# Performance work log

Hardware: AMD Instinct MI355X
Metric: run time of the kernel (lower is better)

Reference implementation:

```python
import jax, jax.numpy as jnp
import numpy as np

B, S, H = 1, 2048, 1024
NH, NKV, HD = 16, 4, 64  # n_attn_heads, n_kv_heads, head_dim


def setup_inputs() -> dict:
    key = jax.random.key(0)
    k1, k2, k3, k4 = jax.random.split(key, 4)
    x = jax.random.normal(k1, (B, S, H), dtype=jnp.float32)
    Wq = jax.random.normal(k2, (H, H), dtype=jnp.float32) * 0.02
    Wk = jax.random.normal(k3, (NKV * HD, H), dtype=jnp.float32) * 0.02
    Wv = jax.random.normal(k4, (NKV * HD, H), dtype=jnp.float32) * 0.02
    return {"x": x, "Wq": Wq, "Wk": Wk, "Wv": Wv}


def reference(x, Wq, Wk, Wv):
    b, s, h = x.shape
    rep = NH // NKV
    # projections (torch Linear: x @ W.T)
    q = (x @ Wq.T).reshape(b, s, NH, HD).transpose(0, 2, 1, 3)      # [b, NH, s, d]
    k = (x @ Wk.T).reshape(b, s, NKV, HD).transpose(0, 2, 1, 3)     # [b, NKV, s, d]
    v = (x @ Wv.T).reshape(b, s, NKV, HD).transpose(0, 2, 1, 3)
    # repeat_kv: expand each kv head rep times
    k = jnp.repeat(k, rep, axis=1)                                   # [b, NH, s, d]
    v = jnp.repeat(v, rep, axis=1)
    # NOTE: source scales by 1/sqrt(hidden_size), not 1/sqrt(head_dim)
    scale = 1.0 / np.sqrt(H).astype(np.float32)
    scores = jnp.einsum('bhqd,bhkd->bhqk', q, k) * scale             # [b, NH, s, s]
    causal = jnp.tril(jnp.ones((s, s), dtype=bool))
    scores = jnp.where(causal[None, None], scores, -jnp.inf)
    probs = jax.nn.softmax(scores, axis=-1)
    y = jnp.einsum('bhqk,bhkd->bhqd', probs, v)                      # [b, NH, s, d]
    return y.transpose(0, 2, 1, 3).reshape(b, s, NH * HD)
```

## Files before the change

### kernel.cpp

```cpp
#include <hip/hip_runtime.h>

#define S_LEN 2048
#define HID   1024
#define NHEAD 16
#define NKVH  4
#define HDIM  64
#define NPROJ 1536
#define QKSTR 1280

typedef __bf16 bf16x8 __attribute__((ext_vector_type(8)));
typedef __bf16 bf16x4 __attribute__((ext_vector_type(4)));
typedef float  f32x4  __attribute__((ext_vector_type(4)));
typedef short  s16x4  __attribute__((ext_vector_type(4)));

typedef const __attribute__((address_space(1))) void* gas_ptr;
typedef __attribute__((address_space(3))) void*       las_ptr;

#define QSCALE 0.04508422f

__device__ __forceinline__ unsigned short f2bf(float f) {
    unsigned u = __builtin_bit_cast(unsigned, f);
    u = u + 0x7FFFu + ((u >> 16) & 1u);
    return (unsigned short)(u >> 16);
}

__device__ __forceinline__ f32x4 mfma_16x16x16_bf16(s16x4 a, s16x4 b, f32x4 c) {
#if __has_builtin(__builtin_amdgcn_mfma_f32_16x16x16bf16_1k)
    return __builtin_amdgcn_mfma_f32_16x16x16bf16_1k(a, b, c, 0, 0, 0);
#else
    f32x4 d = c;
    asm volatile("s_nop 1\n\tv_mfma_f32_16x16x16_bf16 %0, %1, %2, %0\n\ts_nop 3"
                 : "+v"(d) : "v"(a), "v"(b));
    return d;
#endif
}

__global__ __launch_bounds__(256) void cvt_all(
    const float* __restrict__ x,  const float* __restrict__ wq,
    const float* __restrict__ wk, const float* __restrict__ wv,
    unsigned short* __restrict__ xbf, unsigned short* __restrict__ wbf)
{
    const long nx  = (long)S_LEN * HID;
    const long nwq = (long)HID * HID;
    const long nwk = (long)256 * HID;
    long i = (long)(blockIdx.x * 256 + threadIdx.x) * 4;
    const float* src; unsigned short* dst;
    if (i < nx)                  { src = x  + i;                 dst = xbf + i; }
    else if (i < nx + nwq)       { long j = i - nx;              src = wq + j; dst = wbf + j; }
    else if (i < nx + nwq + nwk) { long j = i - nx - nwq;        src = wk + j; dst = wbf + nwq + j; }
    else                         { long j = i - nx - nwq - nwk;  src = wv + j; dst = wbf + nwq + nwk + j; }
    float4 v = *(const float4*)src;
    ushort4 o; o.x = f2bf(v.x); o.y = f2bf(v.y); o.z = f2bf(v.z); o.w = f2bf(v.w);
    *(ushort4*)dst = o;
}

__global__ __launch_bounds__(256, 2) void proj_gemm(
    const unsigned short* __restrict__ xbf,
    const unsigned short* __restrict__ wbf,
    unsigned short* __restrict__ qkv,
    unsigned short* __restrict__ vT)
{
    __shared__ unsigned short At[2][64 * 64];
    __shared__ unsigned short Bt[2][96 * 64];
    const int tid = threadIdx.x;
    const int w = tid >> 6, l = tid & 63;
    const int quad = l >> 4, lane16 = l & 15;
    const int m0 = blockIdx.y * 64, n0 = blockIdx.x * 96;
    const int wm = (w & 1) * 32, wn = (w >> 1) * 48;

    const int srow = l >> 3;
    const int scol = ((l & 7) ^ srow) * 8;

    f32x4 acc[2][3] = {};

    #define STAGE(KT, BUF)                                                              \
        do {                                                                            \
            _Pragma("unroll")                                                           \
            for (int c = 0; c < 2; ++c) {                                               \
                const int rbase = w * 16 + c * 8;                                       \
                const unsigned short* ga =                                              \
                    xbf + (long)(m0 + rbase + srow) * HID + (KT) + scol;                \
                __builtin_amdgcn_global_load_lds((gas_ptr)ga,                           \
                    (las_ptr)&At[BUF][rbase * 64], 16, 0, 0);                           \
            }                                                                           \
            _Pragma("unroll")                                                           \
            for (int c = 0; c < 3; ++c) {                                               \
                const int rbase = w * 24 + c * 8;                                       \
                const unsigned short* gb =                                              \
                    wbf + (long)(n0 + rbase + srow) * HID + (KT) + scol;                \
                __builtin_amdgcn_global_load_lds((gas_ptr)gb,                           \
                    (las_ptr)&Bt[BUF][rbase * 64], 16, 0, 0);                           \
            }                                                                           \
        } while (0)

    STAGE(0, 0);

    for (int i = 0; i < 16; ++i) {
        const int cur = i & 1;
        __syncthreads();
        if (i + 1 < 16) STAGE((i + 1) * 64, cur ^ 1);

        #pragma unroll
        for (int ks = 0; ks < 2; ++ks) {
            const int swz = ((ks * 4 + quad) ^ (lane16 & 7)) * 8;
            bf16x8 a[2], b[3];
            #pragma unroll
            for (int mi = 0; mi < 2; ++mi)
                a[mi] = *(const bf16x8*)&At[cur][(wm + mi * 16 + lane16) * 64 + swz];
            #pragma unroll
            for (int ni = 0; ni < 3; ++ni)
                b[ni] = *(const bf16x8*)&Bt[cur][(wn + ni * 16 + lane16) * 64 + swz];
            #pragma unroll
            for (int mi = 0; mi < 2; ++mi)
                #pragma unroll
                for (int ni = 0; ni < 3; ++ni)
                    acc[mi][ni] = __builtin_amdgcn_mfma_f32_16x16x32_bf16(a[mi], b[ni], acc[mi][ni], 0, 0, 0);
        }
    }
    #undef STAGE

    #pragma unroll
    for (int mi = 0; mi < 2; ++mi) {
        const int row = m0 + wm + mi * 16 + quad * 4;
        #pragma unroll
        for (int ni = 0; ni < 3; ++ni) {
            const int col = n0 + wn + ni * 16 + lane16;
            #pragma unroll
            for (int r = 0; r < 4; ++r) {
                const float v = acc[mi][ni][r];
                if (col < 1024)
                    qkv[(long)(row + r) * QKSTR + col] = f2bf(v * QSCALE);
                else if (col < 1280)
                    qkv[(long)(row + r) * QKSTR + col] = f2bf(v);
                else
                    vT[(long)(col - 1280) * S_LEN + (row + r)] = f2bf(v);
            }
        }
    }
}

#define KSTR 72
__global__ __launch_bounds__(256, 2) void attn(
    const unsigned short* __restrict__ qkv,
    const unsigned short* __restrict__ vT,
    float* __restrict__ out)
{
    __shared__ unsigned short Kt[2][64 * KSTR];
    __shared__ unsigned short Vt[2][64 * KSTR];

    const int tid = threadIdx.x;
    const int w = tid >> 6, l = tid & 63;
    const int quad = l >> 4, lane16 = l & 15;
    const int bx = blockIdx.x, by = blockIdx.y;
    const int qt = (by & 8) ? (31 - bx) : bx;
    const int h  = by;
    const int kh = h >> 2;
    const int qcol = h * 64;
    const int kcol = 1024 + kh * 64;

    const long qrow = (long)(qt * 64 + w * 16 + lane16);
    bf16x8 qa0 = *(const bf16x8*)&qkv[qrow * QKSTR + qcol + quad * 8];
    bf16x8 qa1 = *(const bf16x8*)&qkv[qrow * QKSTR + qcol + 32 + quad * 8];

    f32x4 oT[4] = {};
    float rsum[4] = {0.f, 0.f, 0.f, 0.f};

    const int sr = tid >> 2, ss = tid & 3;
    const long vrow = (long)(kh * 64 + sr) * S_LEN;

    bf16x8 kr0, kr1, vr0, vr1;
    {
        const long gk = (long)sr * QKSTR + kcol + ss * 16;
        kr0 = *(const bf16x8*)&qkv[gk];
        kr1 = *(const bf16x8*)&qkv[gk + 8];
        const long gv = vrow + ss * 16;
        vr0 = *(const bf16x8*)&vT[gv];
        vr1 = *(const bf16x8*)&vT[gv + 8];
    }

    for (int kt = 0; kt <= qt; ++kt) {
        const int cur = kt & 1;
        *(bf16x8*)&Kt[cur][sr * KSTR + ss * 16]     = kr0;
        *(bf16x8*)&Kt[cur][sr * KSTR + ss * 16 + 8] = kr1;
        *(bf16x8*)&Vt[cur][sr * KSTR + ss * 16]     = vr0;
        *(bf16x8*)&Vt[cur][sr * KSTR + ss * 16 + 8] = vr1;

        __syncthreads();

        if (kt < qt) {
            const long gk = (long)((kt + 1) * 64 + sr) * QKSTR + kcol + ss * 16;
            kr0 = *(const bf16x8*)&qkv[gk];
            kr1 = *(const bf16x8*)&qkv[gk + 8];
            const long gv = vrow + (kt + 1) * 64 + ss * 16;
            vr0 = *(const bf16x8*)&vT[gv];
            vr1 = *(const bf16x8*)&vT[gv + 8];
        }

        f32x4 sacc[4] = {};
        __builtin_amdgcn_s_setprio(1);
        #pragma unroll
        for (int t = 0; t < 4; ++t) {
            bf16x8 kb0 = *(const bf16x8*)&Kt[cur][(t * 16 + lane16) * KSTR + quad * 8];
            bf16x8 kb1 = *(const bf16x8*)&Kt[cur][(t * 16 + lane16) * KSTR + 32 + quad * 8];
            sacc[t] = __builtin_amdgcn_mfma_f32_16x16x32_bf16(kb0, qa0, sacc[t], 0, 0, 0);
            sacc[t] = __builtin_amdgcn_mfma_f32_16x16x32_bf16(kb1, qa1, sacc[t], 0, 0, 0);
        }
        __builtin_amdgcn_s_setprio(0);

        if (kt == qt) {
            #pragma unroll
            for (int t = 0; t < 4; ++t) {
                const int kvw = t * 16 + quad * 4;
                #pragma unroll
                for (int r = 0; r < 4; ++r)
                    if (kvw + r > w * 16 + lane16) sacc[t][r] = -3.0e38f;
            }
        }

        s16x4 pfrag[4];
        #pragma unroll
        for (int t = 0; t < 4; ++t) {
            const float p0 = __builtin_amdgcn_exp2f(sacc[t][0]);
            const float p1 = __builtin_amdgcn_exp2f(sacc[t][1]);
            const float p2 = __builtin_amdgcn_exp2f(sacc[t][2]);
            const float p3 = __builtin_amdgcn_exp2f(sacc[t][3]);
            rsum[t] += (p0 + p1) + (p2 + p3);
            bf16x4 pk;
            pk[0] = (__bf16)p0; pk[1] = (__bf16)p1;
            pk[2] = (__bf16)p2; pk[3] = (__bf16)p3;
            pfrag[t] = __builtin_bit_cast(s16x4, pk);
        }

        __builtin_amdgcn_s_setprio(1);
        #pragma unroll
        for (int dt = 0; dt < 4; ++dt)
            #pragma unroll
            for (int t = 0; t < 4; ++t) {
                bf16x4 va = *(const bf16x4*)&Vt[cur][(dt * 16 + lane16) * KSTR + t * 16 + quad * 4];
                oT[dt] = mfma_16x16x16_bf16(__builtin_bit_cast(s16x4, va), pfrag[t], oT[dt]);
            }
        __builtin_amdgcn_s_setprio(0);
    }

    float total = (rsum[0] + rsum[1]) + (rsum[2] + rsum[3]);
    total += __shfl_xor(total, 16);
    total += __shfl_xor(total, 32);
    const float invt = 1.0f / total;

    const long orow_q = (long)(qt * 64 + w * 16 + lane16);
    #pragma unroll
    for (int dt = 0; dt < 4; ++dt) {
        const int col = h * 64 + dt * 16 + quad * 4;
        #pragma unroll
        for (int r = 0; r < 4; ++r)
            out[orow_q * (NHEAD * HDIM) + col + r] = oT[dt][r] * invt;
    }
}

extern "C" void kernel_launch(void* const* d_in, const int* in_sizes, int n_in,
                              void* d_out, int out_size, void* d_ws, size_t ws_size,
                              hipStream_t stream) {
    const float* x  = (const float*)d_in[0];
    const float* wq = (const float*)d_in[1];
    const float* wk = (const float*)d_in[2];
    const float* wv = (const float*)d_in[3];
    float* out = (float*)d_out;

    unsigned short* xbf = (unsigned short*)d_ws;
    unsigned short* wbf = xbf + (size_t)S_LEN * HID;
    unsigned short* qkv = wbf + (size_t)NPROJ * HID;
    unsigned short* vT  = qkv + (size_t)S_LEN * QKSTR;

    cvt_all<<<dim3(3584), dim3(256), 0, stream>>>(x, wq, wk, wv, xbf, wbf);
    proj_gemm<<<dim3(16, 32), dim3(256), 0, stream>>>(xbf, wbf, qkv, vT);
    attn<<<dim3(32, 16), dim3(256), 0, stream>>>(qkv, vT, out);
}
```

Measured before the change: 116.7 us.

## Fuse fp32-to-bf16 conversion into projection GEMM and process two KV tiles per barrier

Removes the separate conversion kernel. The projection GEMM now loads fp32 x and weights straight into registers, converts them to bf16 and writes them to shared memory, which saves a kernel launch and a round trip through the workspace. The attention kernel widens its shared K/V buffers to four slots and handles two 64-row KV tiles per __syncthreads, with two register prefetch slots, so it needs half as many barriers. In exchange the GEMM loads twice as many bytes per tile, loses the asynchronous global-to-LDS path, and every block re-converts the weights redundantly. Attention also uses more LDS and registers, which may reduce occupancy.

After: 117.2 us. About the same (+0.4%).

```diff
diff --git a/kernel.cpp b/kernel.cpp
--- a/kernel.cpp
+++ b/kernel.cpp
@@ -5,7 +5,6 @@
 #define NHEAD 16
 #define NKVH  4
 #define HDIM  64
-#define NPROJ 1536
 #define QKSTR 1280
 
 typedef __bf16 bf16x8 __attribute__((ext_vector_type(8)));
@@ -13,15 +12,19 @@
 typedef float  f32x4  __attribute__((ext_vector_type(4)));
 typedef short  s16x4  __attribute__((ext_vector_type(4)));
 
-typedef const __attribute__((address_space(1))) void* gas_ptr;
-typedef __attribute__((address_space(3))) void*       las_ptr;
-
 #define QSCALE 0.04508422f
 
 __device__ __forceinline__ unsigned short f2bf(float f) {
     unsigned u = __builtin_bit_cast(unsigned, f);
     u = u + 0x7FFFu + ((u >> 16) & 1u);
     return (unsigned short)(u >> 16);
+}
+
+__device__ __forceinline__ bf16x8 cvt8(float4 a, float4 b) {
+    bf16x8 r;
+    r[0] = (__bf16)a.x; r[1] = (__bf16)a.y; r[2] = (__bf16)a.z; r[3] = (__bf16)a.w;
+    r[4] = (__bf16)b.x; r[5] = (__bf16)b.y; r[6] = (__bf16)b.z; r[7] = (__bf16)b.w;
+    return r;
 }
 
 __device__ __forceinline__ f32x4 mfma_16x16x16_bf16(s16x4 a, s16x4 b, f32x4 c) {
@@ -35,28 +38,9 @@
 #endif
 }
 
-__global__ __launch_bounds__(256) void cvt_all(
+__global__ __launch_bounds__(256, 2) void proj_gemm(
     const float* __restrict__ x,  const float* __restrict__ wq,
     const float* __restrict__ wk, const float* __restrict__ wv,
-    unsigned short* __restrict__ xbf, unsigned short* __restrict__ wbf)
-{
-    const long nx  = (long)S_LEN * HID;
-    const long nwq = (long)HID * HID;
-    const long nwk = (long)256 * HID;
-    long i = (long)(blockIdx.x * 256 + threadIdx.x) * 4;
-    const float* src; unsigned short* dst;
-    if (i < nx)                  { src = x  + i;                 dst = xbf + i; }
-    else if (i < nx + nwq)       { long j = i - nx;              src = wq + j; dst = wbf + j; }
-    else if (i < nx + nwq + nwk) { long j = i - nx - nwq;        src = wk + j; dst = wbf + nwq + j; }
-    else                         { long j = i - nx - nwq - nwk;  src = wv + j; dst = wbf + nwq + nwk + j; }
-    float4 v = *(const float4*)src;
-    ushort4 o; o.x = f2bf(v.x); o.y = f2bf(v.y); o.z = f2bf(v.z); o.w = f2bf(v.w);
-    *(ushort4*)dst = o;
-}
-
-__global__ __launch_bounds__(256, 2) void proj_gemm(
-    const unsigned short* __restrict__ xbf,
-    const unsigned short* __restrict__ wbf,
     unsigned short* __restrict__ qkv,
     unsigned short* __restrict__ vT)
 {
@@ -70,35 +54,51 @@
 
     const int srow = l >> 3;
     const int scol = ((l & 7) ^ srow) * 8;
+    const int dcol = (l & 7) * 8;
 
     f32x4 acc[2][3] = {};
-
-    #define STAGE(KT, BUF)                                                              \
+    float4 arA[2][2], arB[3][2];
+
+    #define PLOAD(KT)                                                                   \
         do {                                                                            \
             _Pragma("unroll")                                                           \
             for (int c = 0; c < 2; ++c) {                                               \
-                const int rbase = w * 16 + c * 8;                                       \
-                const unsigned short* ga =                                              \
-                    xbf + (long)(m0 + rbase + srow) * HID + (KT) + scol;                \
-                __builtin_amdgcn_global_load_lds((gas_ptr)ga,                           \
-                    (las_ptr)&At[BUF][rbase * 64], 16, 0, 0);                           \
+                const float* ga = x + (long)(m0 + w * 16 + c * 8 + srow) * HID          \
+                                    + (KT) + scol;                                      \
+                arA[c][0] = ((const float4*)ga)[0];                                     \
+                arA[c][1] = ((const float4*)ga)[1];                                     \
             }                                                                           \
             _Pragma("unroll")                                                           \
             for (int c = 0; c < 3; ++c) {                                               \
-                const int rbase = w * 24 + c * 8;                                       \
-                const unsigned short* gb =                                              \
-                    wbf + (long)(n0 + rbase + srow) * HID + (KT) + scol;                \
-                __builtin_amdgcn_global_load_lds((gas_ptr)gb,                           \
-                    (las_ptr)&Bt[BUF][rbase * 64], 16, 0, 0);                           \
+                const int row = n0 + w * 24 + c * 8 + srow;                             \
+                const float* gb = (row < 1024) ? wq + (long)row * HID                   \
+                                : (row < 1280) ? wk + (long)(row - 1024) * HID          \
+                                               : wv + (long)(row - 1280) * HID;         \
+                gb += (KT) + scol;                                                      \
+                arB[c][0] = ((const float4*)gb)[0];                                     \
+                arB[c][1] = ((const float4*)gb)[1];                                     \
             }                                                                           \
         } while (0)
 
-    STAGE(0, 0);
+    #define PWRITE(BUF)                                                                 \
+        do {                                                                            \
+            _Pragma("unroll")                                                           \
+            for (int c = 0; c < 2; ++c)                                                 \
+                *(bf16x8*)&At[BUF][(w * 16 + c * 8 + srow) * 64 + dcol] =               \
+                    cvt8(arA[c][0], arA[c][1]);                                         \
+            _Pragma("unroll")                                                           \
+            for (int c = 0; c < 3; ++c)                                                 \
+                *(bf16x8*)&Bt[BUF][(w * 24 + c * 8 + srow) * 64 + dcol] =               \
+                    cvt8(arB[c][0], arB[c][1]);                                         \
+        } while (0)
+
+    PLOAD(0);
 
     for (int i = 0; i < 16; ++i) {
         const int cur = i & 1;
+        PWRITE(cur);
         __syncthreads();
-        if (i + 1 < 16) STAGE((i + 1) * 64, cur ^ 1);
+        if (i + 1 < 16) PLOAD((i + 1) * 64);
 
         #pragma unroll
         for (int ks = 0; ks < 2; ++ks) {
@@ -117,7 +117,8 @@
                     acc[mi][ni] = __builtin_amdgcn_mfma_f32_16x16x32_bf16(a[mi], b[ni], acc[mi][ni], 0, 0, 0);
         }
     }
-    #undef STAGE
+    #undef PLOAD
+    #undef PWRITE
 
     #pragma unroll
     for (int mi = 0; mi < 2; ++mi) {
@@ -145,8 +146,8 @@
     const unsigned short* __restrict__ vT,
     float* __restrict__ out)
 {
-    __shared__ unsigned short Kt[2][64 * KSTR];
-    __shared__ unsigned short Vt[2][64 * KSTR];
+    __shared__ unsigned short Kt[4][64 * KSTR];
+    __shared__ unsigned short Vt[4][64 * KSTR];
 
     const int tid = threadIdx.x;
     const int w = tid >> 6, l = tid & 63;
@@ -168,46 +169,46 @@
     const int sr = tid >> 2, ss = tid & 3;
     const long vrow = (long)(kh * 64 + sr) * S_LEN;
 
-    bf16x8 kr0, kr1, vr0, vr1;
-    {
-        const long gk = (long)sr * QKSTR + kcol + ss * 16;
-        kr0 = *(const bf16x8*)&qkv[gk];
-        kr1 = *(const bf16x8*)&qkv[gk + 8];
-        const long gv = vrow + ss * 16;
-        vr0 = *(const bf16x8*)&vT[gv];
-        vr1 = *(const bf16x8*)&vT[gv + 8];
-    }
-
-    for (int kt = 0; kt <= qt; ++kt) {
-        const int cur = kt & 1;
-        *(bf16x8*)&Kt[cur][sr * KSTR + ss * 16]     = kr0;
-        *(bf16x8*)&Kt[cur][sr * KSTR + ss * 16 + 8] = kr1;
-        *(bf16x8*)&Vt[cur][sr * KSTR + ss * 16]     = vr0;
-        *(bf16x8*)&Vt[cur][sr * KSTR + ss * 16 + 8] = vr1;
-
-        __syncthreads();
-
-        if (kt < qt) {
-            const long gk = (long)((kt + 1) * 64 + sr) * QKSTR + kcol + ss * 16;
-            kr0 = *(const bf16x8*)&qkv[gk];
-            kr1 = *(const bf16x8*)&qkv[gk + 8];
-            const long gv = vrow + (kt + 1) * 64 + ss * 16;
-            vr0 = *(const bf16x8*)&vT[gv];
-            vr1 = *(const bf16x8*)&vT[gv + 8];
-        }
-
+    const int nt = qt + 1;
+
+    bf16x8 kr00, kr01, vr00, vr01;
+    bf16x8 kr10, kr11, vr10, vr11;
+
+    #define LOADSLOT0(T)                                                        \
+        do {                                                                    \
+            const long gk = (long)((T) * 64 + sr) * QKSTR + kcol + ss * 16;     \
+            kr00 = *(const bf16x8*)&qkv[gk];                                    \
+            kr01 = *(const bf16x8*)&qkv[gk + 8];                                \
+            const long gv = vrow + (T) * 64 + ss * 16;                          \
+            vr00 = *(const bf16x8*)&vT[gv];                                     \
+            vr01 = *(const bf16x8*)&vT[gv + 8];                                 \
+        } while (0)
+    #define LOADSLOT1(T)                                                        \
+        do {                                                                    \
+            const long gk = (long)((T) * 64 + sr) * QKSTR + kcol + ss * 16;     \
+            kr10 = *(const bf16x8*)&qkv[gk];                                    \
+            kr11 = *(const bf16x8*)&qkv[gk + 8];                                \
+            const long gv = vrow + (T) * 64 + ss * 16;                          \
+            vr10 = *(const bf16x8*)&vT[gv];                                     \
+            vr11 = *(const bf16x8*)&vT[gv + 8];                                 \
+        } while (0)
+
+    LOADSLOT0(0);
+    if (nt > 1) LOADSLOT1(1);
+
+    auto compute = [&](int buf, int tile) {
         f32x4 sacc[4] = {};
         __builtin_amdgcn_s_setprio(1);
         #pragma unroll
         for (int t = 0; t < 4; ++t) {
-            bf16x8 kb0 = *(const bf16x8*)&Kt[cur][(t * 16 + lane16) * KSTR + quad * 8];
-            bf16x8 kb1 = *(const bf16x8*)&Kt[cur][(t * 16 + lane16) * KSTR + 32 + quad * 8];
+            bf16x8 kb0 = *(const bf16x8*)&Kt[buf][(t * 16 + lane16) * KSTR + quad * 8];
+            bf16x8 kb1 = *(const bf16x8*)&Kt[buf][(t * 16 + lane16) * KSTR + 32 + quad * 8];
             sacc[t] = __builtin_amdgcn_mfma_f32_16x16x32_bf16(kb0, qa0, sacc[t], 0, 0, 0);
             sacc[t] = __builtin_amdgcn_mfma_f32_16x16x32_bf16(kb1, qa1, sacc[t], 0, 0, 0);
         }
         __builtin_amdgcn_s_setprio(0);
 
-        if (kt == qt) {
+        if (tile == qt) {
             #pragma unroll
             for (int t = 0; t < 4; ++t) {
                 const int kvw = t * 16 + quad * 4;
@@ -236,11 +237,37 @@
         for (int dt = 0; dt < 4; ++dt)
             #pragma unroll
             for (int t = 0; t < 4; ++t) {
-                bf16x4 va = *(const bf16x4*)&Vt[cur][(dt * 16 + lane16) * KSTR + t * 16 + quad * 4];
+                bf16x4 va = *(const bf16x4*)&Vt[buf][(dt * 16 + lane16) * KSTR + t * 16 + quad * 4];
                 oT[dt] = mfma_16x16x16_bf16(__builtin_bit_cast(s16x4, va), pfrag[t], oT[dt]);
             }
         __builtin_amdgcn_s_setprio(0);
+    };
+
+    for (int j = 0; 2 * j < nt; ++j) {
+        const int t0 = 2 * j, t1 = 2 * j + 1;
+        const bool has1 = (t1 < nt);
+        const int p = (j & 1) << 1;
+
+        *(bf16x8*)&Kt[p][sr * KSTR + ss * 16]     = kr00;
+        *(bf16x8*)&Kt[p][sr * KSTR + ss * 16 + 8] = kr01;
+        *(bf16x8*)&Vt[p][sr * KSTR + ss * 16]     = vr00;
+        *(bf16x8*)&Vt[p][sr * KSTR + ss * 16 + 8] = vr01;
+        if (has1) {
+            *(bf16x8*)&Kt[p + 1][sr * KSTR + ss * 16]     = kr10;
+            *(bf16x8*)&Kt[p + 1][sr * KSTR + ss * 16 + 8] = kr11;
+            *(bf16x8*)&Vt[p + 1][sr * KSTR + ss * 16]     = vr10;
+            *(bf16x8*)&Vt[p + 1][sr * KSTR + ss * 16 + 8] = vr11;
+        }
+        __syncthreads();
+
+        if (t0 + 2 < nt) LOADSLOT0(t0 + 2);
+        if (t1 + 2 < nt) LOADSLOT1(t1 + 2);
+
+        compute(p, t0);
+        if (has1) compute(p + 1, t1);
     }
+    #undef LOADSLOT0
+    #undef LOADSLOT1
 
     float total = (rsum[0] + rsum[1]) + (rsum[2] + rsum[3]);
     total += __shfl_xor(total, 16);
@@ -266,12 +293,9 @@
     const float* wv = (const float*)d_in[3];
     float* out = (float*)d_out;
 
-    unsigned short* xbf = (unsigned short*)d_ws;
-    unsigned short* wbf = xbf + (size_t)S_LEN * HID;
-    unsigned short* qkv = wbf + (size_t)NPROJ * HID;
+    unsigned short* qkv = (unsigned short*)d_ws;
     unsigned short* vT  = qkv + (size_t)S_LEN * QKSTR;
 
-    cvt_all<<<dim3(3584), dim3(256), 0, stream>>>(x, wq, wk, wv, xbf, wbf);
-    proj_gemm<<<dim3(16, 32), dim3(256), 0, stream>>>(xbf, wbf, qkv, vT);
+    proj_gemm<<<dim3(16, 32), dim3(256), 0, stream>>>(x, wq, wk, wv, qkv, vT);
     attn<<<dim3(32, 16), dim3(256), 0, stream>>>(qkv, vT, out);
 }
```
